# Kernel tuning notes

Hardware: AMD Instinct MI355X
Metric: run time of the kernel (lower is better)

Reference implementation:

```python
import jax, jax.numpy as jnp
import numpy as np
from jax import lax

B = 128

# ---- 4-qubit statevector helpers (RY + CNOT circuit is real-valued) ----

def _init_state(n):
    s = jnp.zeros((n, 2, 2, 2, 2), jnp.float32)
    return s.at[:, 0, 0, 0, 0].set(1.0)


def _ry(state, theta, wire):
    # RY(t) = [[cos t/2, -sin t/2],[sin t/2, cos t/2]]; theta: scalar or [N]
    s = jnp.moveaxis(state, wire + 1, 1)
    c = jnp.cos(theta * 0.5)
    sn = jnp.sin(theta * 0.5)
    if jnp.ndim(theta) > 0:
        c = c.reshape(-1, 1, 1, 1)
        sn = sn.reshape(-1, 1, 1, 1)
    a, b = s[:, 0], s[:, 1]
    s = jnp.stack([c * a - sn * b, sn * a + c * b], axis=1)
    return jnp.moveaxis(s, 1, wire + 1)


def _cnot(state, ctrl, tgt):
    s = jnp.moveaxis(state, [ctrl + 1, tgt + 1], [1, 2])
    s = jnp.concatenate([s[:, :1], jnp.flip(s[:, 1:], axis=2)], axis=1)
    return jnp.moveaxis(s, [1, 2], [ctrl + 1, tgt + 1])


def _random_layer(state, thetas):
    for i in range(4):
        state = _ry(state, thetas[i], i)
        state = _cnot(state, i, (i + 1) % 4)
    return state


def _measure_z(state, wire):
    p = jnp.moveaxis(state, wire + 1, 1) ** 2
    p = p.reshape(p.shape[0], 2, -1).sum(-1)
    return p[:, 0] - p[:, 1]


def setup_inputs() -> dict:
    key = jax.random.key(0)
    ks = jax.random.split(key, 12)

    def n(k, shape, scale):
        return jax.random.normal(k, shape, jnp.float32) * scale

    return {
        "x": jax.random.normal(ks[0], (B, 3, 249, 249), jnp.float32),
        "conv1_w": n(ks[1], (6, 3, 5, 5), 0.1),
        "conv1_b": jnp.zeros((6,), jnp.float32),
        "conv2_w": n(ks[2], (15, 6, 3, 3), 0.1),
        "conv2_b": jnp.zeros((15,), jnp.float32),
        "fc1_w": n(ks[3], (120, 55815), 1.0 / np.sqrt(55815.0)),
        "fc1_b": jnp.zeros((120,), jnp.float32),
        "fc2_w": n(ks[4], (84, 120), 1.0 / np.sqrt(120.0)),
        "fc2_b": jnp.zeros((84,), jnp.float32),
        "fc3_w": n(ks[5], (1, 84), 1.0 / np.sqrt(84.0)),
        "fc3_b": jnp.zeros((1,), jnp.float32),
        "head_thetas": jax.random.uniform(ks[6], (4,), jnp.float32, 0.0, 2.0 * np.pi),
        "qf_thetas": jax.random.uniform(ks[7], (4,), jnp.float32, 0.0, 2.0 * np.pi),
        "lin_w": n(ks[8], (1, 784), 1.0 / np.sqrt(784.0)),
        "lin_b": jnp.zeros((1,), jnp.float32),
    }


def reference(x, conv1_w, conv1_b, conv2_w, conv2_b, fc1_w, fc1_b, fc2_w, fc2_b,
              fc3_w, fc3_b, head_thetas, qf_thetas, lin_w, lin_b):
    bsz = x.shape[0]

    def conv(y, w, b, stride):
        y = lax.conv_general_dilated(y, w, (stride, stride), [(1, 1), (1, 1)],
                                     dimension_numbers=("NCHW", "OIHW", "NCHW"))
        return y + b[None, :, None, None]

    def pool(y):  # MaxPool2d(kernel=2, stride=1)
        return lax.reduce_window(y, -jnp.inf, lax.max, (1, 1, 2, 2), (1, 1, 1, 1), "VALID")

    # ---- conv branch (dropout = identity in eval) ----
    h = pool(jax.nn.relu(conv(x, conv1_w, conv1_b, 2)))          # [B,6,123,123]
    h = pool(jax.nn.relu(conv(h, conv2_w, conv2_b, 2)))          # [B,15,61,61]
    h = h.reshape(bsz, -1)                                        # [B,55815]
    h = jax.nn.relu(h @ fc1_w.T + fc1_b)
    h = jax.nn.relu(h @ fc2_w.T + fc2_b)
    logit = (h @ fc3_w.T + fc3_b)[:, 0]                           # [B]
    st = _init_state(bsz)
    st = _ry(st, logit, 0)
    st = _random_layer(st, head_thetas)
    probs_conv = jax.nn.sigmoid(_measure_z(st, 0))[:, None]       # [B,1]

    # ---- quanvolution branch ----
    gray = x.mean(axis=1, keepdims=True)                          # [B,1,249,249]
    g = jax.image.resize(gray, (bsz, 1, 28, 28), method="linear")[:, 0]
    # 2x2 patches, row-major, element order [tl, tr, bl, br]
    patches = g.reshape(bsz, 14, 2, 14, 2).transpose(0, 1, 3, 2, 4).reshape(bsz * 196, 4)
    st = _init_state(bsz * 196)
    for w in range(4):
        st = _ry(st, patches[:, w], w)
    st = _random_layer(st, qf_thetas)
    feats = jnp.stack([_measure_z(st, w) for w in range(4)], axis=1).reshape(bsz, 784)
    probs_q = jax.nn.sigmoid(feats @ lin_w.T + lin_b)             # [B,1]

    probs = (probs_conv + probs_q) * 0.5
    return jnp.concatenate([probs, 1.0 - probs], axis=-1)         # [B,2]
```

## Files before the change

kernel.cpp:

```cpp
#include <hip/hip_runtime.h>
#include <math.h>

#define DEV static __device__ __forceinline__

template <int W>
DEV void q_ry(float s[16], float th) {
  float c = cosf(th * 0.5f), sn = sinf(th * 0.5f);
  constexpr int m = 8 >> W;
#pragma unroll
  for (int i = 0; i < 16; ++i) {
    if (!(i & m)) {
      float a = s[i], b = s[i | m];
      s[i] = c * a - sn * b;
      s[i | m] = sn * a + c * b;
    }
  }
}
template <int C, int T>
DEV void q_cnot(float s[16]) {
  constexpr int mc = 8 >> C, mt = 8 >> T;
#pragma unroll
  for (int i = 0; i < 16; ++i) {
    if ((i & mc) && !(i & mt)) {
      float t = s[i]; s[i] = s[i | mt]; s[i | mt] = t;
    }
  }
}
template <int W>
DEV float q_mz(const float s[16]) {
  constexpr int m = 8 >> W;
  float p = 0.f;
#pragma unroll
  for (int i = 0; i < 16; ++i) p += (i & m) ? -s[i] * s[i] : s[i] * s[i];
  return p;
}
DEV void q_layer(float s[16], const float* __restrict__ th) {
  q_ry<0>(s, th[0]); q_cnot<0, 1>(s);
  q_ry<1>(s, th[1]); q_cnot<1, 2>(s);
  q_ry<2>(s, th[2]); q_cnot<2, 3>(s);
  q_ry<3>(s, th[3]); q_cnot<3, 0>(s);
}

__global__ void k_wre(const float* __restrict__ c1w, float* __restrict__ wre1) {
  int t = blockIdx.x * 256 + threadIdx.x;
  if (t < 450) {
    int g = t / 30, rem = t % 30;
    int ci = g / 5, ky = g % 5, kx = rem / 6, co = rem % 6;
    wre1[t] = c1w[co * 75 + ci * 25 + ky * 5 + kx];
  }
}

DEV int c1_rowbase(int row) { return row * 39 + ((row >> 1) & 1); }

__global__ __launch_bounds__(256, 4) void k_conv1(const float* __restrict__ x,
                                                  const float* __restrict__ wre1,
                                                  const float* __restrict__ bia,
                                                  float* __restrict__ out) {
  __shared__ float smem[4800];
  float (*ct)[42][19] = (float (*)[42][19])smem;
  int b = blockIdx.z;
  int PY0 = blockIdx.y * 41, PX0 = blockIdx.x * 16;
  int iy0 = PY0 * 2 - 1, ix0 = PX0 * 2 - 1;
  int tid = threadIdx.x;
  const float* xb = x + (size_t)b * 186003;
  int r = tid / 6, seg = tid - 6 * (tid / 6);
  float acc[6][3];
#pragma unroll
  for (int co = 0; co < 6; ++co) {
    float bv = bia[co];
#pragma unroll
    for (int c = 0; c < 3; ++c) acc[co][c] = bv;
  }
#pragma unroll 1
  for (int ci = 0; ci < 3; ++ci) {
    if (ci) __syncthreads();
    const float* xci = xb + ci * 62001;
#pragma unroll
    for (int s = 0; s < 14; ++s) {
      int idx = s * 256 + tid;
      bool ok = idx < 3393;
      int rr = idx / 39, cc = idx - rr * 39;
      int iy = iy0 + rr, ix = ix0 + cc;
      float v = 0.f;
      if (ok && cc < 37 && (unsigned)iy < 249u && (unsigned)ix < 249u)
        v = xci[iy * 249 + ix];
      if (ok && cc < 37) smem[c1_rowbase(rr) + cc] = v;
    }
    __syncthreads();
    if (tid < 252) {
#pragma unroll
      for (int ky = 0; ky < 5; ++ky) {
        const float* xrow = &smem[c1_rowbase(2 * r + ky) + 6 * seg];
        float xv[10];
#pragma unroll
        for (int j = 0; j < 10; ++j) xv[j] = xrow[j];
        const float* wp = wre1 + (ci * 5 + ky) * 30;
        float wr[30];
#pragma unroll
        for (int j = 0; j < 30; ++j) wr[j] = wp[j];
#pragma unroll
        for (int c = 0; c < 3; ++c)
#pragma unroll
          for (int kx = 0; kx < 5; ++kx)
#pragma unroll
            for (int co = 0; co < 6; ++co)
              acc[co][c] += xv[2 * c + kx] * wr[kx * 6 + co];
      }
    }
  }
  __syncthreads();
  if (tid < 252) {
#pragma unroll
    for (int co = 0; co < 6; ++co)
#pragma unroll
      for (int c = 0; c < 3; ++c)
        if (3 * seg + c < 17) ct[co][r][3 * seg + c] = acc[co][c];
  }
  __syncthreads();
#pragma unroll
  for (int co2 = 0; co2 < 6; ++co2) {
    for (int j = tid; j < 41 * 16; j += 256) {
      int pr = j >> 4, pc = j & 15;
      float m = fmaxf(fmaxf(ct[co2][pr][pc], ct[co2][pr][pc + 1]),
                      fmaxf(ct[co2][pr + 1][pc], ct[co2][pr + 1][pc + 1]));
      out[((size_t)(b * 6 + co2) * 123 + PY0 + pr) * 128 + PX0 + pc] = fmaxf(m, 0.f);
    }
  }
}

__global__ __launch_bounds__(256, 4) void k_conv2(const float* __restrict__ in,
                                                  const float* __restrict__ w,
                                                  const float* __restrict__ bia,
                                                  float* __restrict__ out) {
  __shared__ float smem[6 * 35 * 36];
  float (*xs)[35][36] = (float (*)[35][36])smem;
  float (*ct)[17][18] = (float (*)[17][18])smem;
  int b = blockIdx.z;
  int py0 = blockIdx.y * 16, px0 = blockIdx.x * 16;
  int iy0 = py0 * 2 - 1, ix0 = px0 * 2 - 1;
  int tid = threadIdx.x;
  const float* ib = in + (size_t)b * 94464;
  for (int idx = tid; idx < 6 * 35 * 36; idx += 256) {
    int ci = idx / 1260, rem = idx % 1260, rr = rem / 36, cc = rem % 36;
    int iy = iy0 + rr, ix = ix0 + cc;
    float v = 0.f;
    if (cc < 35 && (unsigned)iy < 123u && (unsigned)ix < 123u)
      v = ib[ci * 15744 + iy * 128 + ix];
    xs[ci][rr][cc] = v;
  }
  __syncthreads();
  int co = tid % 15, ty = tid / 15;
  float acc[17];
  if (tid < 255) {
    float bv = bia[co];
#pragma unroll
    for (int t = 0; t < 17; ++t) acc[t] = bv;
#pragma unroll
    for (int ci = 0; ci < 6; ++ci) {
      float wreg[9];
#pragma unroll
      for (int j = 0; j < 9; ++j) wreg[j] = w[co * 54 + ci * 9 + j];
#pragma unroll
      for (int ky = 0; ky < 3; ++ky) {
        const float* xrow = &xs[ci][2 * ty + ky][0];
        float xv[36];
#pragma unroll
        for (int j = 0; j < 18; ++j) {
          float2 t2 = *reinterpret_cast<const float2*>(&xrow[2 * j]);
          xv[2 * j] = t2.x; xv[2 * j + 1] = t2.y;
        }
#pragma unroll
        for (int tx = 0; tx < 17; ++tx)
#pragma unroll
          for (int kx = 0; kx < 3; ++kx)
            acc[tx] += xv[2 * tx + kx] * wreg[ky * 3 + kx];
      }
    }
  }
  __syncthreads();
  if (tid < 255) {
#pragma unroll
    for (int tx = 0; tx < 17; ++tx) ct[co][ty][tx] = acc[tx];
  }
  __syncthreads();
  for (int i = tid; i < 15 * 16 * 16; i += 256) {
    int co2 = i / 256, rem = i % 256, pr = rem / 16, pc = rem % 16;
    int py = py0 + pr, px = px0 + pc;
    if (py < 61 && px < 61) {
      float m = fmaxf(fmaxf(ct[co2][pr][pc], ct[co2][pr][pc + 1]),
                      fmaxf(ct[co2][pr + 1][pc], ct[co2][pr + 1][pc + 1]));
      out[(size_t)b * 55815 + co2 * 3721 + py * 61 + px] = fmaxf(m, 0.f);
    }
  }
}

#define KFC 55815
#define NCHUNK 1745
#define FC1_BLOCKS 512
__global__ __launch_bounds__(256) void k_fc1(const float* __restrict__ h,
                                             const float* __restrict__ w,
                                             float* __restrict__ partial) {
  __shared__ float hs[128][33];
  __shared__ float wsd[120][33];
  int tid = threadIdx.x;
  int tb = tid & 31;
  int bo = tid >> 5;
  float acc[4][15];
#pragma unroll
  for (int j = 0; j < 4; ++j)
#pragma unroll
    for (int oo = 0; oo < 15; ++oo) acc[j][oo] = 0.f;

  for (int ch = blockIdx.x; ch < NCHUNK; ch += FC1_BLOCKS) {
    int k0 = ch * 32;
    for (int idx = tid; idx < 128 * 32; idx += 256) {
      int bb = idx >> 5, kk = idx & 31;
      int k = k0 + kk;
      hs[bb][kk] = (k < KFC) ? h[(size_t)bb * KFC + k] : 0.f;
    }
    for (int idx = tid; idx < 120 * 32; idx += 256) {
      int oo = idx >> 5, kk = idx & 31;
      int k = k0 + kk;
      wsd[oo][kk] = (k < KFC) ? w[(size_t)oo * KFC + k] : 0.f;
    }
    __syncthreads();
#pragma unroll 4
    for (int kk = 0; kk < 32; ++kk) {
      float hv[4], wv[15];
#pragma unroll
      for (int j = 0; j < 4; ++j) hv[j] = hs[tb + 32 * j][kk];
#pragma unroll
      for (int oo = 0; oo < 15; ++oo) wv[oo] = wsd[bo * 15 + oo][kk];
#pragma unroll
      for (int j = 0; j < 4; ++j)
#pragma unroll
        for (int oo = 0; oo < 15; ++oo) acc[j][oo] += hv[j] * wv[oo];
    }
    __syncthreads();
  }
  float* pg = partial + (size_t)blockIdx.x * 15360;
#pragma unroll
  for (int j = 0; j < 4; ++j) {
    int b = tb + 32 * j;
#pragma unroll
    for (int oo = 0; oo < 15; ++oo) pg[b * 120 + bo * 15 + oo] = acc[j][oo];
  }
}

__global__ __launch_bounds__(256) void k_fc1_reduce(const float* __restrict__ partial,
                                                    const float* __restrict__ bias,
                                                    float* __restrict__ outv) {
  int i = blockIdx.x * 256 + threadIdx.x;
  if (i >= 15360) return;
  float a = bias[i % 120];
  for (int g = 0; g < FC1_BLOCKS; ++g) a += partial[(size_t)g * 15360 + i];
  outv[i] = fmaxf(a, 0.f);
}

__global__ __launch_bounds__(128) void k_head(const float* __restrict__ fc1o,
                                              const float* __restrict__ w2,
                                              const float* __restrict__ b2,
                                              const float* __restrict__ w3,
                                              const float* __restrict__ b3,
                                              const float* __restrict__ hth,
                                              float* __restrict__ probs_conv) {
  __shared__ float h1[120];
  __shared__ float h2[84];
  int b = blockIdx.x, tid = threadIdx.x;
  if (tid < 120) h1[tid] = fc1o[b * 120 + tid];
  __syncthreads();
  if (tid < 84) {
    float a = b2[tid];
    for (int k = 0; k < 120; ++k) a += h1[k] * w2[tid * 120 + k];
    h2[tid] = fmaxf(a, 0.f);
  }
  __syncthreads();
  if (tid == 0) {
    float lg = b3[0];
    for (int j = 0; j < 84; ++j) lg += h2[j] * w3[j];
    float s[16];
#pragma unroll
    for (int i = 0; i < 16; ++i) s[i] = 0.f;
    s[0] = 1.f;
    q_ry<0>(s, lg);
    q_layer(s, hth);
    float z = q_mz<0>(s);
    probs_conv[b] = 1.f / (1.f + expf(-z));
  }
}

DEV void resize_win(int o, int& i0, int& i1, float& sf, float& inorm) {
  const float invs = 249.0f / 28.0f;
  sf = ((float)o + 0.5f) * invs - 0.5f;
  i0 = (int)ceilf(sf - invs); if (i0 < 0) i0 = 0;
  i1 = (int)floorf(sf + invs); if (i1 > 248) i1 = 248;
  float nrm = 0.f;
  for (int i = i0; i <= i1; ++i)
    nrm += fmaxf(0.f, 1.f - fabsf(sf - (float)i) * (28.0f / 249.0f));
  inorm = 1.f / nrm;
}

__global__ __launch_bounds__(256) void k_resize1(const float* __restrict__ x,
                                                 float* __restrict__ tmp) {
  __shared__ float accs[4][28][64];
  __shared__ float sf_t[28], inorm_t[28];
  int b = blockIdx.x >> 2, cg = blockIdx.x & 3;
  int tid = threadIdx.x;
  int iysub = tid >> 6, lane = tid & 63;
  int col = cg * 64 + lane;
  bool colok = col < 249;
  for (int i = tid; i < 4 * 28 * 64; i += 256) ((float*)accs)[i] = 0.f;
  if (tid < 28) {
    int i0, i1; float sf, inm;
    resize_win(tid, i0, i1, sf, inm);
    sf_t[tid] = sf; inorm_t[tid] = inm;
  }
  __syncthreads();
  const float* xb = x + (size_t)b * 186003;
  const float S = 28.0f / 249.0f;
  for (int it = 0; it < 63; ++it) {
    int iy = it * 4 + iysub;
    if (iy < 249 && colok) {
      int off = iy * 249 + col;
      float gray = (xb[off] + xb[62001 + off] + xb[124002 + off]) * (1.0f / 3.0f);
      float u = ((float)iy + 0.5f) * S;
      int oyh = (int)floorf(u + 0.5f);
#pragma unroll
      for (int d = 0; d < 2; ++d) {
        int oy = oyh - d;
        if (oy >= 0 && oy < 28) {
          float wv = fmaxf(0.f, 1.f - fabsf(sf_t[oy] - (float)iy) * S) * inorm_t[oy];
          accs[iysub][oy][lane] += wv * gray;
        }
      }
    }
  }
  __syncthreads();
  for (int i = tid; i < 28 * 64; i += 256) {
    int oy = i >> 6, c2 = i & 63;
    int colw = cg * 64 + c2;
    if (colw < 249)
      tmp[((size_t)b * 28 + oy) * 249 + colw] =
          accs[0][oy][c2] + accs[1][oy][c2] + accs[2][oy][c2] + accs[3][oy][c2];
  }
}

__global__ __launch_bounds__(256) void k_quanv(const float* __restrict__ tmp,
                                               const float* __restrict__ qth,
                                               const float* __restrict__ lw,
                                               float* __restrict__ qpart) {
  __shared__ float g[392];
  __shared__ float red[4];
  int bid = blockIdx.x;
  int b = bid >> 1, half = bid & 1;
  int tid = threadIdx.x;
  for (int idx = tid; idx < 392; idx += 256) {
    int ly = idx / 28, ox = idx % 28;
    int oy = 14 * half + ly;
    int i0, i1; float sf, inorm;
    resize_win(ox, i0, i1, sf, inorm);
    const float* tr = tmp + ((size_t)b * 28 + oy) * 249;
    float acc = 0.f;
    for (int i = i0; i <= i1; ++i)
      acc += fmaxf(0.f, 1.f - fabsf(sf - (float)i) * (28.0f / 249.0f)) * inorm * tr[i];
    g[idx] = acc;
  }
  __syncthreads();
  float part = 0.f;
  if (tid < 98) {
    int pl = tid / 14, pj = tid % 14;
    int pi = 7 * half + pl;
    float v0 = g[(2 * pl) * 28 + 2 * pj];
    float v1 = g[(2 * pl) * 28 + 2 * pj + 1];
    float v2 = g[(2 * pl + 1) * 28 + 2 * pj];
    float v3 = g[(2 * pl + 1) * 28 + 2 * pj + 1];
    float s[16];
#pragma unroll
    for (int i = 0; i < 16; ++i) s[i] = 0.f;
    s[0] = 1.f;
    q_ry<0>(s, v0); q_ry<1>(s, v1); q_ry<2>(s, v2); q_ry<3>(s, v3);
    q_layer(s, qth);
    float z0 = q_mz<0>(s), z1 = q_mz<1>(s), z2 = q_mz<2>(s), z3 = q_mz<3>(s);
    const float* lwp = lw + (pi * 14 + pj) * 4;
    part = z0 * lwp[0] + z1 * lwp[1] + z2 * lwp[2] + z3 * lwp[3];
  }
#pragma unroll
  for (int off = 32; off > 0; off >>= 1) part += __shfl_down(part, off, 64);
  if ((tid & 63) == 0) red[tid >> 6] = part;
  __syncthreads();
  if (tid == 0) qpart[bid] = red[0] + red[1] + red[2] + red[3];
}

__global__ __launch_bounds__(128) void k_final(const float* __restrict__ qpart,
                                               const float* __restrict__ lb,
                                               const float* __restrict__ probs_conv,
                                               float* __restrict__ out) {
  int b = threadIdx.x;
  float tot = qpart[2 * b] + qpart[2 * b + 1] + lb[0];
  float pq = 1.f / (1.f + expf(-tot));
  float pr = 0.5f * (probs_conv[b] + pq);
  out[b * 2 + 0] = pr;
  out[b * 2 + 1] = 1.f - pr;
}

extern "C" void kernel_launch(void* const* d_in, const int* in_sizes, int n_in,
                              void* d_out, int out_size, void* d_ws, size_t ws_size,
                              hipStream_t stream) {
  const float* x   = (const float*)d_in[0];
  const float* c1w = (const float*)d_in[1];
  const float* c1b = (const float*)d_in[2];
  const float* c2w = (const float*)d_in[3];
  const float* c2b = (const float*)d_in[4];
  const float* f1w = (const float*)d_in[5];
  const float* f1b = (const float*)d_in[6];
  const float* f2w = (const float*)d_in[7];
  const float* f2b = (const float*)d_in[8];
  const float* f3w = (const float*)d_in[9];
  const float* f3b = (const float*)d_in[10];
  const float* hth = (const float*)d_in[11];
  const float* qth = (const float*)d_in[12];
  const float* lw  = (const float*)d_in[13];
  const float* lb  = (const float*)d_in[14];
  float* out = (float*)d_out;
  char* ws = (char*)d_ws;

  float* pool1   = (float*)(ws);
  float* partial = (float*)(ws);
  float* tmp     = (float*)(ws + 33554432);
  float* h       = (float*)(ws + 48365568);
  float* fc1o    = (float*)(ws + 76942848);
  float* pconv   = (float*)(ws + 77004288);
  float* wre1    = (float*)(ws + 77004800);
  float* qpart   = (float*)(ws + 77009848);

  k_wre<<<dim3(2), 256, 0, stream>>>(c1w, wre1);
  k_conv1<<<dim3(8, 3, 128), 256, 0, stream>>>(x, wre1, c1b, pool1);
  k_conv2<<<dim3(4, 4, 128), 256, 0, stream>>>(pool1, c2w, c2b, h);
  k_fc1<<<dim3(FC1_BLOCKS), 256, 0, stream>>>(h, f1w, partial);
  k_fc1_reduce<<<dim3(60), 256, 0, stream>>>(partial, f1b, fc1o);
  k_head<<<dim3(128), 128, 0, stream>>>(fc1o, f2w, f2b, f3w, f3b, hth, pconv);
  k_resize1<<<dim3(512), 256, 0, stream>>>(x, tmp);
  k_quanv<<<dim3(256), 256, 0, stream>>>(tmp, qth, lw, qpart);
  k_final<<<dim3(1), 128, 0, stream>>>(qpart, lb, pconv, out);
}
```

Measured before the change: 268.6 us.

## Double-buffer conv1 input, split fc1 reduction in two stages, widen resize grid

The conv1 kernel now prefetches the next input channel into registers while computing the current one, then stores it into a second shared-memory buffer. This hides global-load latency and removes one barrier per channel, at the cost of more LDS and registers. The fc1 partial-sum reduction, previously 60 blocks each looping over all FC1_BLOCKS partials, becomes a two-stage reduction with 960 blocks followed by a small final pass, to expose more parallelism. The resize kernel uses 32-column tiles with 8 row-subgroups, doubling its block count. The two-stage reduction assumes FC1_BLOCKS equals 512.

After: 271.1 us. About the same (+0.9%).

```diff
diff --git a/kernel.cpp b/kernel.cpp
--- a/kernel.cpp
+++ b/kernel.cpp
@@ -56,7 +56,7 @@
                                                   const float* __restrict__ wre1,
                                                   const float* __restrict__ bia,
                                                   float* __restrict__ out) {
-  __shared__ float smem[4800];
+  __shared__ float smem[6800];
   float (*ct)[42][19] = (float (*)[42][19])smem;
   int b = blockIdx.z;
   int PY0 = blockIdx.y * 41, PX0 = blockIdx.x * 16;
@@ -71,10 +71,8 @@
 #pragma unroll
     for (int c = 0; c < 3; ++c) acc[co][c] = bv;
   }
-#pragma unroll 1
-  for (int ci = 0; ci < 3; ++ci) {
-    if (ci) __syncthreads();
-    const float* xci = xb + ci * 62001;
+  {
+    const float* xci = xb;
 #pragma unroll
     for (int s = 0; s < 14; ++s) {
       int idx = s * 256 + tid;
@@ -86,11 +84,30 @@
         v = xci[iy * 249 + ix];
       if (ok && cc < 37) smem[c1_rowbase(rr) + cc] = v;
     }
-    __syncthreads();
+  }
+  __syncthreads();
+#pragma unroll
+  for (int ci = 0; ci < 3; ++ci) {
+    float vreg[14];
+    if (ci < 2) {
+      const float* xci = xb + (ci + 1) * 62001;
+#pragma unroll
+      for (int s = 0; s < 14; ++s) {
+        int idx = s * 256 + tid;
+        bool ok = idx < 3393;
+        int rr = idx / 39, cc = idx - rr * 39;
+        int iy = iy0 + rr, ix = ix0 + cc;
+        float v = 0.f;
+        if (ok && cc < 37 && (unsigned)iy < 249u && (unsigned)ix < 249u)
+          v = xci[iy * 249 + ix];
+        vreg[s] = v;
+      }
+    }
+    const float* buf = smem + (ci & 1) * 3400;
     if (tid < 252) {
 #pragma unroll
       for (int ky = 0; ky < 5; ++ky) {
-        const float* xrow = &smem[c1_rowbase(2 * r + ky) + 6 * seg];
+        const float* xrow = &buf[c1_rowbase(2 * r + ky) + 6 * seg];
         float xv[10];
 #pragma unroll
         for (int j = 0; j < 10; ++j) xv[j] = xrow[j];
@@ -107,8 +124,18 @@
               acc[co][c] += xv[2 * c + kx] * wr[kx * 6 + co];
       }
     }
-  }
-  __syncthreads();
+    if (ci < 2) {
+      float* nbuf = smem + ((ci + 1) & 1) * 3400;
+#pragma unroll
+      for (int s = 0; s < 14; ++s) {
+        int idx = s * 256 + tid;
+        bool ok = idx < 3393;
+        int rr = idx / 39, cc = idx - rr * 39;
+        if (ok && cc < 37) nbuf[c1_rowbase(rr) + cc] = vreg[s];
+      }
+    }
+    __syncthreads();
+  }
   if (tid < 252) {
 #pragma unroll
     for (int co = 0; co < 6; ++co)
@@ -247,13 +274,25 @@
   }
 }
 
-__global__ __launch_bounds__(256) void k_fc1_reduce(const float* __restrict__ partial,
-                                                    const float* __restrict__ bias,
-                                                    float* __restrict__ outv) {
+__global__ __launch_bounds__(256) void k_reduceA(const float* __restrict__ partial,
+                                                 float* __restrict__ partial2) {
+  int gs = blockIdx.x / 60;
+  int blk = blockIdx.x % 60;
+  int i = blk * 256 + threadIdx.x;
+  float a = 0.f;
+#pragma unroll 8
+  for (int g = gs * 32; g < gs * 32 + 32; ++g)
+    a += partial[(size_t)g * 15360 + i];
+  partial2[(size_t)gs * 15360 + i] = a;
+}
+
+__global__ __launch_bounds__(256) void k_reduceB(const float* __restrict__ partial2,
+                                                 const float* __restrict__ bias,
+                                                 float* __restrict__ outv) {
   int i = blockIdx.x * 256 + threadIdx.x;
-  if (i >= 15360) return;
   float a = bias[i % 120];
-  for (int g = 0; g < FC1_BLOCKS; ++g) a += partial[(size_t)g * 15360 + i];
+#pragma unroll
+  for (int gs = 0; gs < 16; ++gs) a += partial2[(size_t)gs * 15360 + i];
   outv[i] = fmaxf(a, 0.f);
 }
 
@@ -302,14 +341,14 @@
 
 __global__ __launch_bounds__(256) void k_resize1(const float* __restrict__ x,
                                                  float* __restrict__ tmp) {
-  __shared__ float accs[4][28][64];
+  __shared__ float accs[8][28][32];
   __shared__ float sf_t[28], inorm_t[28];
-  int b = blockIdx.x >> 2, cg = blockIdx.x & 3;
+  int b = blockIdx.x >> 3, cg = blockIdx.x & 7;
   int tid = threadIdx.x;
-  int iysub = tid >> 6, lane = tid & 63;
-  int col = cg * 64 + lane;
+  int iysub = tid >> 5, lane = tid & 31;
+  int col = cg * 32 + lane;
   bool colok = col < 249;
-  for (int i = tid; i < 4 * 28 * 64; i += 256) ((float*)accs)[i] = 0.f;
+  for (int i = tid; i < 8 * 28 * 32; i += 256) ((float*)accs)[i] = 0.f;
   if (tid < 28) {
     int i0, i1; float sf, inm;
     resize_win(tid, i0, i1, sf, inm);
@@ -318,8 +357,8 @@
   __syncthreads();
   const float* xb = x + (size_t)b * 186003;
   const float S = 28.0f / 249.0f;
-  for (int it = 0; it < 63; ++it) {
-    int iy = it * 4 + iysub;
+  for (int it = 0; it < 32; ++it) {
+    int iy = it * 8 + iysub;
     if (iy < 249 && colok) {
       int off = iy * 249 + col;
       float gray = (xb[off] + xb[62001 + off] + xb[124002 + off]) * (1.0f / 3.0f);
@@ -336,12 +375,15 @@
     }
   }
   __syncthreads();
-  for (int i = tid; i < 28 * 64; i += 256) {
-    int oy = i >> 6, c2 = i & 63;
-    int colw = cg * 64 + c2;
-    if (colw < 249)
-      tmp[((size_t)b * 28 + oy) * 249 + colw] =
-          accs[0][oy][c2] + accs[1][oy][c2] + accs[2][oy][c2] + accs[3][oy][c2];
+  for (int i = tid; i < 28 * 32; i += 256) {
+    int oy = i >> 5, c2 = i & 31;
+    int colw = cg * 32 + c2;
+    if (colw < 249) {
+      float a = 0.f;
+#pragma unroll
+      for (int u2 = 0; u2 < 8; ++u2) a += accs[u2][oy][c2];
+      tmp[((size_t)b * 28 + oy) * 249 + colw] = a;
+    }
   }
 }
 
@@ -424,22 +466,24 @@
   float* out = (float*)d_out;
   char* ws = (char*)d_ws;
 
-  float* pool1   = (float*)(ws);
-  float* partial = (float*)(ws);
-  float* tmp     = (float*)(ws + 33554432);
-  float* h       = (float*)(ws + 48365568);
-  float* fc1o    = (float*)(ws + 76942848);
-  float* pconv   = (float*)(ws + 77004288);
-  float* wre1    = (float*)(ws + 77004800);
-  float* qpart   = (float*)(ws + 77009848);
+  float* pool1    = (float*)(ws);
+  float* partial  = (float*)(ws);
+  float* tmp      = (float*)(ws + 33554432);
+  float* h        = (float*)(ws + 48365568);
+  float* fc1o     = (float*)(ws + 76942848);
+  float* pconv    = (float*)(ws + 77004288);
+  float* wre1     = (float*)(ws + 77004800);
+  float* qpart    = (float*)(ws + 77009848);
+  float* partial2 = (float*)(ws + 77012992);
 
   k_wre<<<dim3(2), 256, 0, stream>>>(c1w, wre1);
   k_conv1<<<dim3(8, 3, 128), 256, 0, stream>>>(x, wre1, c1b, pool1);
   k_conv2<<<dim3(4, 4, 128), 256, 0, stream>>>(pool1, c2w, c2b, h);
   k_fc1<<<dim3(FC1_BLOCKS), 256, 0, stream>>>(h, f1w, partial);
-  k_fc1_reduce<<<dim3(60), 256, 0, stream>>>(partial, f1b, fc1o);
+  k_reduceA<<<dim3(960), 256, 0, stream>>>(partial, partial2);
+  k_reduceB<<<dim3(60), 256, 0, stream>>>(partial2, f1b, fc1o);
   k_head<<<dim3(128), 128, 0, stream>>>(fc1o, f2w, f2b, f3w, f3b, hth, pconv);
-  k_resize1<<<dim3(512), 256, 0, stream>>>(x, tmp);
+  k_resize1<<<dim3(1024), 256, 0, stream>>>(x, tmp);
   k_quanv<<<dim3(256), 256, 0, stream>>>(tmp, qth, lw, qpart);
   k_final<<<dim3(1), 128, 0, stream>>>(qpart, lb, pconv, out);
 }
```
